# Kernel optimization log

Hardware: AMD Instinct MI355X
Metric: run time of the kernel (lower is better)

## Reference

```python
import jax, jax.numpy as jnp
import numpy as np

D, H, L, P, NQ, B, DFF = 256, 8, 4, 4, 900, 4, 1024
SHAPES = [(128, 128), (64, 64), (32, 32), (16, 16)]
S = sum(h * w for h, w in SHAPES)  # 21760
HD = D // H


def setup_inputs() -> dict:
    key = jax.random.key(0)
    ks = iter(jax.random.split(key, 32))
    r = lambda sh, s=1.0: jax.random.normal(next(ks), sh, jnp.float32) * s
    return dict(
        tgt=r((B, NQ, D)),
        query_pos=r((B, NQ, D)),
        reference_points=jax.random.uniform(next(ks), (B, NQ, L, 2), jnp.float32),
        memory=r((B, S, D)),
        in_proj_w=r((D, 3 * D), 0.02), in_proj_b=jnp.zeros(3 * D, jnp.float32),
        out_proj_w=r((D, D), 0.02), out_proj_b=jnp.zeros(D, jnp.float32),
        ln1_g=jnp.ones(D, jnp.float32), ln1_b=jnp.zeros(D, jnp.float32),
        ln2_g=jnp.ones(D, jnp.float32), ln2_b=jnp.zeros(D, jnp.float32),
        ln3_g=jnp.ones(D, jnp.float32), ln3_b=jnp.zeros(D, jnp.float32),
        vproj_w=r((D, D), 0.02), vproj_b=jnp.zeros(D, jnp.float32),
        off_w=r((D, H * L * P * 2), 0.02), off_b=r((H * L * P * 2,), 0.5),
        aw_w=r((D, H * L * P), 0.02), aw_b=jnp.zeros(H * L * P, jnp.float32),
        oproj_w=r((D, D), 0.02), oproj_b=jnp.zeros(D, jnp.float32),
        lin1_w=r((D, DFF), 0.02), lin1_b=jnp.zeros(DFF, jnp.float32),
        lin2_w=r((DFF, D), 0.02), lin2_b=jnp.zeros(D, jnp.float32),
        spatial_shapes=np.array(SHAPES, np.int32),
        mem_mask=jnp.zeros((B, S), bool),
    )


def _ln(x, g, b):
    m = jnp.mean(x, -1, keepdims=True)
    v = jnp.mean((x - m) ** 2, -1, keepdims=True)
    return (x - m) * jax.lax.rsqrt(v + 1e-5) * g + b


def reference(tgt, query_pos, reference_points, memory,
              in_proj_w, in_proj_b, out_proj_w, out_proj_b,
              ln1_g, ln1_b, ln2_g, ln2_b, ln3_g, ln3_b,
              vproj_w, vproj_b, off_w, off_b, aw_w, aw_b, oproj_w, oproj_b,
              lin1_w, lin1_b, lin2_w, lin2_b, spatial_shapes, mem_mask):
    shapes = np.asarray(spatial_shapes)  # static level shapes

    # ---- self attention (nn.MultiheadAttention, q=k=tgt+pos, v=tgt) ----
    qp = tgt + query_pos
    q = qp @ in_proj_w[:, :D] + in_proj_b[:D]
    k = qp @ in_proj_w[:, D:2 * D] + in_proj_b[D:2 * D]
    v = tgt @ in_proj_w[:, 2 * D:] + in_proj_b[2 * D:]
    split = lambda x: x.reshape(B, NQ, H, HD).transpose(0, 2, 1, 3)
    qh, kh, vh = split(q), split(k), split(v)
    att = jax.nn.softmax(jnp.einsum('bhqd,bhkd->bhqk', qh, kh) / np.sqrt(HD).astype(np.float32), -1)
    sa = jnp.einsum('bhqk,bhkd->bhqd', att, vh).transpose(0, 2, 1, 3).reshape(B, NQ, D)
    tgt = _ln(tgt + sa @ out_proj_w + out_proj_b, ln2_g, ln2_b)

    # ---- MSDeformAttn cross attention ----
    query = tgt + query_pos
    value = memory @ vproj_w + vproj_b
    value = jnp.where(mem_mask[..., None], 0.0, value).reshape(B, S, H, HD)
    off = (query @ off_w + off_b).reshape(B, NQ, H, L, P, 2)
    aw = jax.nn.softmax((query @ aw_w + aw_b).reshape(B, NQ, H, L * P), -1).reshape(B, NQ, H, L, P)
    # offset normalizer is (W_l, H_l)
    normalizer = jnp.stack([jnp.asarray(shapes[:, 1]), jnp.asarray(shapes[:, 0])], -1).astype(jnp.float32)
    loc = reference_points[:, :, None, :, None, :] + off / normalizer[None, None, None, :, None, :]

    acc = jnp.zeros((B, NQ, H, HD), tgt.dtype)
    start = 0
    bidx = jnp.arange(B)[:, None, None, None]
    hidx = jnp.arange(H)[None, None, :, None]
    for l in range(L):
        Hl, Wl = int(shapes[l, 0]), int(shapes[l, 1])
        vf = value[:, start:start + Hl * Wl]  # [B, Hl*Wl, H, HD]
        # grid_sample align_corners=False, zero padding: pixel = loc*size - 0.5
        x = loc[:, :, :, l, :, 0] * Wl - 0.5  # [B,NQ,H,P]
        y = loc[:, :, :, l, :, 1] * Hl - 0.5
        x0 = jnp.floor(x); y0 = jnp.floor(y)
        wx = x - x0; wy = y - y0
        x0i = x0.astype(jnp.int32); y0i = y0.astype(jnp.int32)

        def gather(xi, yi):
            valid = (xi >= 0) & (xi < Wl) & (yi >= 0) & (yi < Hl)
            idx = jnp.clip(yi, 0, Hl - 1) * Wl + jnp.clip(xi, 0, Wl - 1)
            g = vf[bidx, idx, hidx]  # [B,NQ,H,P,HD]
            return jnp.where(valid[..., None], g, 0.0)

        samp = (gather(x0i, y0i) * ((1 - wx) * (1 - wy))[..., None]
                + gather(x0i + 1, y0i) * (wx * (1 - wy))[..., None]
                + gather(x0i, y0i + 1) * ((1 - wx) * wy)[..., None]
                + gather(x0i + 1, y0i + 1) * (wx * wy)[..., None])
        acc = acc + (samp * aw[:, :, :, l, :, None]).sum(3)
        start += Hl * Wl

    ca = acc.reshape(B, NQ, D) @ oproj_w + oproj_b
    tgt = _ln(tgt + ca, ln1_g, ln1_b)

    # ---- FFN ----
    ff = jax.nn.relu(tgt @ lin1_w + lin1_b) @ lin2_w + lin2_b
    return _ln(tgt + ff, ln3_g, ln3_b)
```

## Files before the change

kernel.cpp:

```cpp
#include <hip/hip_runtime.h>
#include <hip/hip_bf16.h>

typedef __attribute__((ext_vector_type(8))) short bf16x8;
typedef __attribute__((ext_vector_type(4))) short bf16x4;
typedef __attribute__((ext_vector_type(4))) float f32x4;

#define DEV static __device__ __forceinline__

constexpr int Bc = 4, NQc = 900, Hc = 8, Sc = 21760;
constexpr int M1 = Bc * NQc;
constexpr int NQT = (NQc + 63) / 64;
constexpr int QT16 = (NQc + 15) / 16;
constexpr int QKo = Bc * Hc * 960 * 32;

DEV short f2bf(float f) {
  union { __hip_bfloat16 h; short s; } u;
  u.h = __float2bfloat16(f);
  return u.s;
}
DEV float bf2f(short s) {
  union { short s; __hip_bfloat16 h; } u;
  u.s = s;
  return __bfloat162float(u.h);
}

DEV void pack_body(const float* W, short* Wt, int K, int N, int t) {
  int n = t % N;
  int k4 = (t / N) * 4;
  bf16x4 o;
  o[0] = f2bf(W[(size_t)(k4 + 0) * N + n]);
  o[1] = f2bf(W[(size_t)(k4 + 1) * N + n]);
  o[2] = f2bf(W[(size_t)(k4 + 2) * N + n]);
  o[3] = f2bf(W[(size_t)(k4 + 3) * N + n]);
  *(bf16x4*)&Wt[((size_t)(k4 >> 5) * N + n) * 32 + (k4 & 31)] = o;
}

__global__ __launch_bounds__(256) void pack_all_k(
    const float* w0, short* t0, const float* w1, short* t1,
    const float* w2, short* t2, const float* w3, short* t3,
    const float* w4, short* t4, const float* w5, short* t5) {
  int t = blockIdx.x * 256 + threadIdx.x;
  if (t < 49152) pack_body(w0, t0, 256, 768, t);
  else if (t < 65536) pack_body(w1, t1, 256, 256, t - 49152);
  else if (t < 81920) pack_body(w2, t2, 256, 256, t - 65536);
  else if (t < 98304) pack_body(w3, t3, 256, 256, t - 81920);
  else if (t < 163840) pack_body(w4, t4, 256, 1024, t - 98304);
  else pack_body(w5, t5, 1024, 256, t - 163840);
}

template <int MODE, int ACT, int MT>
__global__ __launch_bounds__(256) void gemmv_k(
    const float* __restrict__ A, const float* __restrict__ A2,
    const short* __restrict__ Wt, const float* __restrict__ bias,
    void* __restrict__ Cv, float* __restrict__ C2, int M, int N, int K,
    const unsigned char* __restrict__ rowmask, const float* __restrict__ g,
    const float* __restrict__ beta, const float* __restrict__ resid,
    const float* __restrict__ qpos, float* __restrict__ out2) {
  constexpr int IT = MT / 16;
  __shared__ short As[MT * 40];
  __shared__ short Ws[256 * 40];
  const int nb = N >> 8;
  const int mb = blockIdx.x / nb, bn = blockIdx.x - mb * nb;
  const int tid = threadIdx.x;
  const int lane = tid & 63, wave = tid >> 6;
  const int l16 = lane & 15, quad = lane >> 4;
  const int sr = (MT == 64) ? (tid >> 2) : (tid >> 3);
  const int sk = (MT == 64) ? ((tid & 3) * 8) : ((tid & 7) * 4);
  const int arow = mb * MT + sr;
  const bool aval = arow < M;
  const bool useA2 = (MODE == 4) ? (bn < 2) : (A2 != nullptr);
  const float* ap = A + (size_t)arow * K + sk;
  const float* ap2 = (A2 ? A2 : A) + (size_t)arow * K + sk;
  const short* wp = Wt + (size_t)(bn * 256 + tid) * 32;
  const size_t wstep = (size_t)N * 32;
  const int KT = K >> 5;

  f32x4 acc[IT][4] = {};
  float4 pa0[2] = {}, pa1[2] = {};
  bf16x8 pw[2][4];

  auto loadA = [&](int s, int it) {
    if (aval) {
      const float* p = ap + it * 32;
      pa0[s] = *(const float4*)p;
      if constexpr (MT == 64) pa1[s] = *(const float4*)(p + 4);
      if (useA2) {
        const float* p2 = ap2 + it * 32;
        float4 q0 = *(const float4*)p2;
        pa0[s].x += q0.x; pa0[s].y += q0.y; pa0[s].z += q0.z; pa0[s].w += q0.w;
        if constexpr (MT == 64) {
          float4 q1 = *(const float4*)(p2 + 4);
          pa1[s].x += q1.x; pa1[s].y += q1.y; pa1[s].z += q1.z; pa1[s].w += q1.w;
        }
      }
    }
  };
  auto loadW = [&](int s, int it) {
    const short* p = wp + (size_t)it * wstep;
    pw[s][0] = *(const bf16x8*)(p + 0);
    pw[s][1] = *(const bf16x8*)(p + 8);
    pw[s][2] = *(const bf16x8*)(p + 16);
    pw[s][3] = *(const bf16x8*)(p + 24);
  };
  auto stage = [&](int s) {
    if constexpr (MT == 64) {
      bf16x8 t;
      t[0] = f2bf(pa0[s].x); t[1] = f2bf(pa0[s].y); t[2] = f2bf(pa0[s].z); t[3] = f2bf(pa0[s].w);
      t[4] = f2bf(pa1[s].x); t[5] = f2bf(pa1[s].y); t[6] = f2bf(pa1[s].z); t[7] = f2bf(pa1[s].w);
      *(bf16x8*)&As[sr * 40 + sk] = t;
    } else {
      bf16x4 t;
      t[0] = f2bf(pa0[s].x); t[1] = f2bf(pa0[s].y); t[2] = f2bf(pa0[s].z); t[3] = f2bf(pa0[s].w);
      *(bf16x4*)&As[sr * 40 + sk] = t;
    }
    short* wd = &Ws[tid * 40];
    *(bf16x8*)(wd + 0) = pw[s][0];
    *(bf16x8*)(wd + 8) = pw[s][1];
    *(bf16x8*)(wd + 16) = pw[s][2];
    *(bf16x8*)(wd + 24) = pw[s][3];
  };
  auto compute = [&]() {
    bf16x8 af[IT], bfr[4];
#pragma unroll
    for (int i = 0; i < IT; i++)
      af[i] = *(const bf16x8*)&As[(i * 16 + l16) * 40 + quad * 8];
#pragma unroll
    for (int j = 0; j < 4; j++)
      bfr[j] = *(const bf16x8*)&Ws[(wave * 64 + j * 16 + l16) * 40 + quad * 8];
#pragma unroll
    for (int i = 0; i < IT; i++)
#pragma unroll
      for (int j = 0; j < 4; j++)
        acc[i][j] = __builtin_amdgcn_mfma_f32_16x16x32_bf16(af[i], bfr[j], acc[i][j], 0, 0, 0);
  };

  loadA(0, 0); loadW(0, 0);
  loadA(1, 1); loadW(1, 1);
  for (int it = 0; it < KT; it += 2) {
    stage(0);
    __syncthreads();
    if (it + 2 < KT) { loadA(0, it + 2); loadW(0, it + 2); }
    compute();
    __syncthreads();
    stage(1);
    __syncthreads();
    if (it + 3 < KT) { loadA(1, it + 3); loadW(1, it + 3); }
    compute();
    __syncthreads();
  }

  if constexpr (MODE == 4) {
    short* base = (short*)Cv;
#pragma unroll
    for (int i = 0; i < IT; i++)
#pragma unroll
      for (int r = 0; r < 4; r++) {
        const int m = mb * MT + i * 16 + quad * 4 + r;
        if (m >= M) continue;
        const int b = m / NQc, q = m - b * NQc;
#pragma unroll
        for (int j = 0; j < 4; j++) {
          const int cl = wave * 64 + j * 16 + l16;
          const float v = acc[i][j][r] + bias[bn * 256 + cl];
          const int h = cl >> 5, ch = cl & 31;
          if (bn == 0) {
            base[((size_t)(b * 8 + h) * 960 + q) * 32 + ch] =
                f2bf(v * 0.17677669529663687f);
          } else if (bn == 1) {
            base[QKo + ((size_t)(b * 8 + h) * 960 + q) * 32 + ch] = f2bf(v);
          } else {
            base[2 * QKo + ((((size_t)(b * 8 + h) * 15 + (q >> 6)) * 32 + ch) * 64 + (q & 63))] = f2bf(v);
          }
        }
      }
  } else if constexpr (MODE == 0) {
#pragma unroll
    for (int i = 0; i < IT; i++)
#pragma unroll
      for (int j = 0; j < 4; j++) {
        const int cl = wave * 64 + j * 16 + l16;
        const int col = bn * 256 + cl;
        const float bb = bias[col];
#pragma unroll
        for (int r = 0; r < 4; r++) {
          const int m = mb * MT + i * 16 + quad * 4 + r;
          if (m < M) {
            float v = acc[i][j][r] + bb;
            if (ACT == 1) v = fmaxf(v, 0.f);
            ((float*)Cv)[(size_t)m * N + col] = v;
          }
        }
      }
  } else {
#pragma unroll
    for (int j = 0; j < 4; j++) {
      const int cl = wave * 64 + j * 16 + l16;
      const float bb = bias[cl];
#pragma unroll
      for (int i = 0; i < IT; i++)
#pragma unroll
        for (int r = 0; r < 4; r++) {
          const int m = mb * MT + i * 16 + quad * 4 + r;
          const float rs = (m < M) ? resid[(size_t)m * 256 + cl] : 0.f;
          acc[i][j][r] += bb + rs;
        }
    }
    float2* pr = (float2*)As;
#pragma unroll
    for (int i = 0; i < IT; i++)
#pragma unroll
      for (int r = 0; r < 4; r++) {
        float s = 0.f, q = 0.f;
#pragma unroll
        for (int j = 0; j < 4; j++) {
          s += acc[i][j][r];
          q += acc[i][j][r] * acc[i][j][r];
        }
#pragma unroll
        for (int d = 1; d < 16; d <<= 1) {
          s += __shfl_xor(s, d);
          q += __shfl_xor(q, d);
        }
        if (l16 == 0) pr[(i * 16 + quad * 4 + r) * 4 + wave] = make_float2(s, q);
      }
    __syncthreads();
#pragma unroll
    for (int i = 0; i < IT; i++)
#pragma unroll
      for (int r = 0; r < 4; r++) {
        const int ml = i * 16 + quad * 4 + r;
        float2 p0 = pr[ml * 4 + 0], p1 = pr[ml * 4 + 1];
        float2 p2 = pr[ml * 4 + 2], p3 = pr[ml * 4 + 3];
        const float sum = p0.x + p1.x + p2.x + p3.x;
        const float sq = p0.y + p1.y + p2.y + p3.y;
        const float mean = sum * (1.f / 256.f);
        const float var = sq * (1.f / 256.f) - mean * mean;
        const float rstd = rsqrtf(var + 1e-5f);
        const int m = mb * MT + ml;
        if (m < M) {
#pragma unroll
          for (int j = 0; j < 4; j++) {
            const int cl = wave * 64 + j * 16 + l16;
            const float o = (acc[i][j][r] - mean) * rstd * g[cl] + beta[cl];
            ((float*)Cv)[(size_t)m * 256 + cl] = o;
            if (out2) out2[(size_t)m * 256 + cl] = o + qpos[(size_t)m * 256 + cl];
          }
        }
      }
  }
}

__global__ __launch_bounds__(256) void gemm_val_k(
    const float* __restrict__ A, const short* __restrict__ Wt,
    const float* __restrict__ bias, short* __restrict__ Cv, int M,
    const unsigned char* __restrict__ rowmask) {
  const int mb = blockIdx.x;
  const int tid = threadIdx.x;
  const int lane = tid & 63, wave = tid >> 6;
  const int l16 = lane & 15, quad = lane >> 4;

  const float* ap = A + (size_t)(mb * 64 + l16) * 256 + quad * 8;
  const short* wp = Wt + (size_t)(wave * 64 + l16) * 32 + quad * 8;

  f32x4 acc[4][4] = {};
  float4 pa[2][4][2];
  bf16x8 pb[2][4];

  auto loadA = [&](int s, int it) {
#pragma unroll
    for (int i = 0; i < 4; i++) {
      const float* p = ap + (size_t)i * (16 * 256) + it * 32;
      pa[s][i][0] = *(const float4*)p;
      pa[s][i][1] = *(const float4*)(p + 4);
    }
  };
  auto loadB = [&](int s, int it) {
#pragma unroll
    for (int j = 0; j < 4; j++)
      pb[s][j] = *(const bf16x8*)(wp + (size_t)(it * 256 + j * 16) * 32);
  };
  auto comp = [&](int s) {
    bf16x8 af[4];
#pragma unroll
    for (int i = 0; i < 4; i++) {
      af[i][0] = f2bf(pa[s][i][0].x);
      af[i][1] = f2bf(pa[s][i][0].y);
      af[i][2] = f2bf(pa[s][i][0].z);
      af[i][3] = f2bf(pa[s][i][0].w);
      af[i][4] = f2bf(pa[s][i][1].x);
      af[i][5] = f2bf(pa[s][i][1].y);
      af[i][6] = f2bf(pa[s][i][1].z);
      af[i][7] = f2bf(pa[s][i][1].w);
    }
#pragma unroll
    for (int i = 0; i < 4; i++)
#pragma unroll
      for (int j = 0; j < 4; j++)
        acc[i][j] = __builtin_amdgcn_mfma_f32_16x16x32_bf16(af[i], pb[s][j], acc[i][j], 0, 0, 0);
  };

  loadA(0, 0); loadB(0, 0);
  loadA(1, 1); loadB(1, 1);
#pragma unroll
  for (int it = 0; it < 8; it += 2) {
    comp(0);
    if (it + 2 < 8) { loadA(0, it + 2); loadB(0, it + 2); }
    comp(1);
    if (it + 3 < 8) { loadA(1, it + 3); loadB(1, it + 3); }
  }

  float bb[4];
#pragma unroll
  for (int j = 0; j < 4; j++) bb[j] = bias[wave * 64 + j * 16 + l16];
#pragma unroll
  for (int i = 0; i < 4; i++)
#pragma unroll
    for (int r = 0; r < 4; r++) {
      const int m = mb * 64 + i * 16 + quad * 4 + r;
      if (m >= M) continue;
      const bool mk = rowmask[m] != 0;
#pragma unroll
      for (int j = 0; j < 4; j++) {
        const int cl = wave * 64 + j * 16 + l16;
        float v = acc[i][j][r] + bb[j];
        if (mk) v = 0.f;
        Cv[(size_t)m * 256 + cl] = f2bf(v);
      }
    }
}

DEV void gemm32_body(const float* __restrict__ A, const float* __restrict__ W,
                     const float* __restrict__ bias, float* __restrict__ C,
                     int M, int N, int K, int bid) {
  __shared__ float Asf[16][64];
  __shared__ float Bsf[16][68];
  const int nb = N >> 6;
  const int bm = bid / nb, bn = bid % nb;
  const int tid = threadIdx.x;
  const int tm = tid >> 4, tn = tid & 15;
  float acc[4][4] = {};

  for (int k0 = 0; k0 < K; k0 += 16) {
    {
      const int m = tid >> 2, kk = (tid & 3) * 4;
      const int row = bm * 64 + m;
      float4 v = (row < M) ? *(const float4*)(A + (size_t)row * K + k0 + kk)
                           : make_float4(0.f, 0.f, 0.f, 0.f);
      Asf[kk + 0][m] = v.x; Asf[kk + 1][m] = v.y;
      Asf[kk + 2][m] = v.z; Asf[kk + 3][m] = v.w;
    }
    {
      const int kk = tid >> 4, n = (tid & 15) * 4;
      float4 v = *(const float4*)(W + (size_t)(k0 + kk) * N + bn * 64 + n);
      *(float4*)&Bsf[kk][n] = v;
    }
    __syncthreads();
#pragma unroll
    for (int kk = 0; kk < 16; kk++) {
      float a[4], b[4];
#pragma unroll
      for (int i = 0; i < 4; i++) a[i] = Asf[kk][tm * 4 + i];
#pragma unroll
      for (int j = 0; j < 4; j++) b[j] = Bsf[kk][tn * 4 + j];
#pragma unroll
      for (int i = 0; i < 4; i++)
#pragma unroll
        for (int j = 0; j < 4; j++) acc[i][j] = fmaf(a[i], b[j], acc[i][j]);
    }
    __syncthreads();
  }
#pragma unroll
  for (int i = 0; i < 4; i++) {
    const int row = bm * 64 + tm * 4 + i;
    if (row >= M) continue;
#pragma unroll
    for (int j = 0; j < 4; j++) {
      const int col = bn * 64 + tn * 4 + j;
      C[(size_t)row * N + col] = acc[i][j] + bias[col];
    }
  }
}

__global__ __launch_bounds__(256) void gemm32_offaw_k(
    const float* __restrict__ query, const float* __restrict__ off_w,
    const float* __restrict__ off_b, float* __restrict__ offb,
    const float* __restrict__ aw_w, const float* __restrict__ aw_b,
    float* __restrict__ awlin) {
  if (blockIdx.x < 228)
    gemm32_body(query, off_w, off_b, offb, M1, 256, 256, blockIdx.x);
  else
    gemm32_body(query, aw_w, aw_b, awlin, M1, 128, 256, blockIdx.x - 228);
}

__global__ __launch_bounds__(128) void attn_k(const short* __restrict__ qbf,
                                              const short* __restrict__ kbf,
                                              const short* __restrict__ vtbf,
                                              float* __restrict__ sa) {
  __shared__ short Pb[2][16 * 72];
  __shared__ float Om[2][16][32];
  __shared__ float Ml[2][16][2];
  const int bid = blockIdx.x;
  const int qt = bid % QT16, bh = bid / QT16;
  const int tid = threadIdx.x, lane = tid & 63, wave = tid >> 6;
  const int l16 = lane & 15, quad = lane >> 4;

  const int q_local = min(qt * 16 + l16, NQc - 1);
  const bf16x8 qf = *(const bf16x8*)&qbf[((size_t)bh * 960 + q_local) * 32 + quad * 8];
  const short* kb = kbf + (size_t)bh * 960 * 32;
  const short* vb = vtbf + (size_t)bh * 15 * 32 * 64;

  f32x4 o0 = {}, o1 = {};
  float mrun[4] = {-1e30f, -1e30f, -1e30f, -1e30f};
  float lrun[4] = {0.f, 0.f, 0.f, 0.f};
  short* pw = Pb[wave];

  for (int kt = wave; kt < NQT; kt += 2) {
    const int k0 = kt * 64;
    f32x4 s[4];
#pragma unroll
    for (int st = 0; st < 4; st++) {
      const int key = k0 + st * 16 + l16;
      const bf16x8 kf = *(const bf16x8*)&kb[(size_t)key * 32 + quad * 8];
      f32x4 z = {};
      s[st] = __builtin_amdgcn_mfma_f32_16x16x32_bf16(qf, kf, z, 0, 0, 0);
      if (key >= NQc) { s[st][0] = -1e30f; s[st][1] = -1e30f; s[st][2] = -1e30f; s[st][3] = -1e30f; }
    }
    float mnew[4], alpha[4];
#pragma unroll
    for (int r = 0; r < 4; r++) {
      float mx = fmaxf(fmaxf(s[0][r], s[1][r]), fmaxf(s[2][r], s[3][r]));
#pragma unroll
      for (int d = 1; d < 16; d <<= 1) mx = fmaxf(mx, __shfl_xor(mx, d));
      mnew[r] = fmaxf(mrun[r], mx);
      alpha[r] = __expf(mrun[r] - mnew[r]);
      mrun[r] = mnew[r];
    }
    float tsum[4] = {0.f, 0.f, 0.f, 0.f};
#pragma unroll
    for (int st = 0; st < 4; st++)
#pragma unroll
      for (int r = 0; r < 4; r++) {
        float p = __expf(s[st][r] - mnew[r]);
        s[st][r] = p;
        tsum[r] += p;
      }
#pragma unroll
    for (int r = 0; r < 4; r++) {
      float t = tsum[r];
#pragma unroll
      for (int d = 1; d < 16; d <<= 1) t += __shfl_xor(t, d);
      lrun[r] = lrun[r] * alpha[r] + t;
      o0[r] *= alpha[r];
      o1[r] *= alpha[r];
    }
#pragma unroll
    for (int st = 0; st < 4; st++)
#pragma unroll
      for (int r = 0; r < 4; r++)
        pw[(quad * 4 + r) * 72 + st * 16 + l16] = f2bf(s[st][r]);
    const short* vt = vb + kt * (32 * 64);
#pragma unroll
    for (int c = 0; c < 2; c++) {
      bf16x8 pf = *(const bf16x8*)&pw[l16 * 72 + c * 32 + quad * 8];
      bf16x8 vf0 = *(const bf16x8*)&vt[(size_t)l16 * 64 + c * 32 + quad * 8];
      bf16x8 vf1 = *(const bf16x8*)&vt[(size_t)(16 + l16) * 64 + c * 32 + quad * 8];
      o0 = __builtin_amdgcn_mfma_f32_16x16x32_bf16(pf, vf0, o0, 0, 0, 0);
      o1 = __builtin_amdgcn_mfma_f32_16x16x32_bf16(pf, vf1, o1, 0, 0, 0);
    }
  }
#pragma unroll
  for (int r = 0; r < 4; r++) {
    Om[wave][quad * 4 + r][l16] = o0[r];
    Om[wave][quad * 4 + r][16 + l16] = o1[r];
  }
  if (l16 == 0) {
#pragma unroll
    for (int r = 0; r < 4; r++) {
      Ml[wave][quad * 4 + r][0] = mrun[r];
      Ml[wave][quad * 4 + r][1] = lrun[r];
    }
  }
  __syncthreads();
  {
    const int q = tid >> 3;
    const int c4 = (tid & 7) * 4;
    const float m0 = Ml[0][q][0], m1 = Ml[1][q][0];
    const float M = fmaxf(m0, m1);
    const float a0 = __expf(m0 - M), a1 = __expf(m1 - M);
    const float lsum = a0 * Ml[0][q][1] + a1 * Ml[1][q][1];
    const int qg = qt * 16 + q;
    if (qg < NQc) {
      const float inv = 1.f / lsum;
      float4 o;
      o.x = (a0 * Om[0][q][c4 + 0] + a1 * Om[1][q][c4 + 0]) * inv;
      o.y = (a0 * Om[0][q][c4 + 1] + a1 * Om[1][q][c4 + 1]) * inv;
      o.z = (a0 * Om[0][q][c4 + 2] + a1 * Om[1][q][c4 + 2]) * inv;
      o.w = (a0 * Om[0][q][c4 + 3] + a1 * Om[1][q][c4 + 3]) * inv;
      const int b = bh >> 3, h = bh & 7;
      *(float4*)&sa[(size_t)(b * NQc + qg) * 256 + h * 32 + c4] = o;
    }
  }
}

__global__ __launch_bounds__(256) void sample_k(
    const float* __restrict__ awlin, const float* __restrict__ off,
    const float* __restrict__ refp, const short* __restrict__ value,
    float* __restrict__ accout) {
  const int wid = blockIdx.x * 4 + (threadIdx.x >> 6);
  const int lane = threadIdx.x & 63;
  const int bq = wid >> 3, h = wid & 7;
  const int b = bq / NQc;
  const int l16 = lane & 15;

  float wraw = awlin[(size_t)bq * 128 + h * 16 + l16];
  float mx = wraw;
#pragma unroll
  for (int d = 1; d < 16; d <<= 1) mx = fmaxf(mx, __shfl_xor(mx, d));
  float e = __expf(wraw - mx), ssum = e;
#pragma unroll
  for (int d = 1; d < 16; d <<= 1) ssum += __shfl_xor(ssum, d);
  const float wnorm = e / ssum;

  const int ch = lane & 31, sub = lane >> 5;
  float facc = 0.f;
#pragma unroll
  for (int it = 0; it < 8; it++) {
    const int pt = it * 2 + sub;
    const float w = __shfl(wnorm, pt);
    const int l = pt >> 2;
    const int W = 128 >> l;
    const int start = (l == 0) ? 0 : (l == 1) ? 16384 : (l == 2) ? 20480 : 21504;
    const float offx = off[(size_t)bq * 256 + h * 32 + pt * 2];
    const float offy = off[(size_t)bq * 256 + h * 32 + pt * 2 + 1];
    const float rx = refp[(size_t)bq * 8 + l * 2];
    const float ry = refp[(size_t)bq * 8 + l * 2 + 1];
    const float x = rx * (float)W + offx - 0.5f;
    const float y = ry * (float)W + offy - 0.5f;
    const float x0f = floorf(x), y0f = floorf(y);
    const float wx = x - x0f, wy = y - y0f;
    const int x0 = (int)x0f, y0 = (int)y0f;
    const short* vbp = value + ((size_t)b * Sc + start) * 256 + h * 32 + ch;
#pragma unroll
    for (int c4 = 0; c4 < 4; c4++) {
      const int dx = c4 & 1, dy = c4 >> 1;
      const int xi = x0 + dx, yi = y0 + dy;
      const bool valid = (xi >= 0) && (xi < W) && (yi >= 0) && (yi < W);
      const int xc = min(max(xi, 0), W - 1);
      const int yc = min(max(yi, 0), W - 1);
      const float gvv = bf2f(vbp[(size_t)(yc * W + xc) * 256]);
      const float ww = (dx ? wx : 1.f - wx) * (dy ? wy : 1.f - wy);
      facc += valid ? w * ww * gvv : 0.f;
    }
  }
  facc += __shfl_xor(facc, 32);
  if (lane < 32) accout[(size_t)bq * 256 + h * 32 + ch] = facc;
}

extern "C" void kernel_launch(void* const* d_in, const int* in_sizes, int n_in,
                              void* d_out, int out_size, void* d_ws,
                              size_t ws_size, hipStream_t stream) {
  const float* tgt = (const float*)d_in[0];
  const float* query_pos = (const float*)d_in[1];
  const float* refp = (const float*)d_in[2];
  const float* memory = (const float*)d_in[3];
  const float* in_proj_w = (const float*)d_in[4];
  const float* in_proj_b = (const float*)d_in[5];
  const float* out_proj_w = (const float*)d_in[6];
  const float* out_proj_b = (const float*)d_in[7];
  const float* ln1_g = (const float*)d_in[8];
  const float* ln1_b = (const float*)d_in[9];
  const float* ln2_g = (const float*)d_in[10];
  const float* ln2_b = (const float*)d_in[11];
  const float* ln3_g = (const float*)d_in[12];
  const float* ln3_b = (const float*)d_in[13];
  const float* vproj_w = (const float*)d_in[14];
  const float* vproj_b = (const float*)d_in[15];
  const float* off_w = (const float*)d_in[16];
  const float* off_b = (const float*)d_in[17];
  const float* aw_w = (const float*)d_in[18];
  const float* aw_b = (const float*)d_in[19];
  const float* oproj_w = (const float*)d_in[20];
  const float* oproj_b = (const float*)d_in[21];
  const float* lin1_w = (const float*)d_in[22];
  const float* lin1_b = (const float*)d_in[23];
  const float* lin2_w = (const float*)d_in[24];
  const float* lin2_b = (const float*)d_in[25];
  const unsigned char* mem_mask = (const unsigned char*)d_in[27];
  float* out = (float*)d_out;

  float* ws = (float*)d_ws;
  short* qbf = (short*)(ws + 921600);
  float* sa = ws + 3686400;
  float* tgt2 = ws + 5529600;
  float* query = ws + 6451200;
  float* offb = ws + 7372800;
  float* awlin = ws + 8294400;
  float* accb = ws + 8755200;
  float* tgt3 = ws + 9676800;
  float* ff1 = ws + 10598400;
  short* valueBf = (short*)(ws + 14284800);
  short* wbase = valueBf + 22282240;
  short* inT = wbase + 0;
  short* outT = wbase + 196608;
  short* vT = wbase + 262144;
  short* oT = wbase + 327680;
  short* lin1T = wbase + 393216;
  short* lin2T = wbase + 655360;

  pack_all_k<<<896, 256, 0, stream>>>(in_proj_w, inT, out_proj_w, outT,
                                      vproj_w, vT, oproj_w, oT,
                                      lin1_w, lin1T, lin2_w, lin2T);

  gemmv_k<4, 0, 32><<<113 * 3, 256, 0, stream>>>(
      tgt, query_pos, inT, in_proj_b, qbf, nullptr, M1, 768, 256,
      nullptr, nullptr, nullptr, nullptr, nullptr, nullptr);
  attn_k<<<Bc * Hc * QT16, 128, 0, stream>>>(qbf, qbf + QKo, qbf + 2 * QKo, sa);
  gemmv_k<3, 0, 32><<<113, 256, 0, stream>>>(
      sa, nullptr, outT, out_proj_b, tgt2, nullptr, M1, 256, 256,
      nullptr, ln2_g, ln2_b, tgt, query_pos, query);
  gemm_val_k<<<1360, 256, 0, stream>>>(memory, vT, vproj_b, valueBf, Bc * Sc, mem_mask);
  gemm32_offaw_k<<<342, 256, 0, stream>>>(query, off_w, off_b, offb, aw_w, aw_b, awlin);
  sample_k<<<Bc * NQc * Hc / 4, 256, 0, stream>>>(awlin, offb, refp, valueBf, accb);
  gemmv_k<3, 0, 32><<<113, 256, 0, stream>>>(
      accb, nullptr, oT, oproj_b, tgt3, nullptr, M1, 256, 256,
      nullptr, ln1_g, ln1_b, tgt2, nullptr, nullptr);
  gemmv_k<0, 1, 64><<<57 * 4, 256, 0, stream>>>(
      tgt3, nullptr, lin1T, lin1_b, ff1, nullptr, M1, 1024, 256,
      nullptr, nullptr, nullptr, nullptr, nullptr, nullptr);
  gemmv_k<3, 0, 32><<<113, 256, 0, stream>>>(
      ff1, nullptr, lin2T, lin2_b, out, nullptr, M1, 256, 1024,
      nullptr, ln3_g, ln3_b, tgt3, nullptr, nullptr);
}
```

Measured before the change: 422.7 us.

## Stage value-projection A tiles into LDS via async global_load_lds with N split

Rewrites the value-projection GEMM so fp32 memory rows are copied directly into a double-buffered, XOR-swizzled LDS tile using global_load_lds, rather than each wave loading them into registers. The N dimension is split across two blocks with a 2x2 wave layout, which doubles the grid and halves the accumulators per wave. An occupancy hint of 4 blocks is added. The aim is to lower register pressure and redundant A traffic and to overlap copies with MFMA work. The cost is syncthreads barriers on every iteration, and each A tile is now read by two blocks.

```diff
diff --git a/kernel.cpp b/kernel.cpp
--- a/kernel.cpp
+++ b/kernel.cpp
@@ -250,28 +250,35 @@
   }
 }
 
-__global__ __launch_bounds__(256) void gemm_val_k(
+__global__ __launch_bounds__(256, 4) void gemm_val_k(
     const float* __restrict__ A, const short* __restrict__ Wt,
     const float* __restrict__ bias, short* __restrict__ Cv, int M,
     const unsigned char* __restrict__ rowmask) {
-  const int mb = blockIdx.x;
+  __shared__ float As[2][64 * 32];
+  const int mb = blockIdx.x >> 1, bn = blockIdx.x & 1;
   const int tid = threadIdx.x;
   const int lane = tid & 63, wave = tid >> 6;
   const int l16 = lane & 15, quad = lane >> 4;
-
-  const float* ap = A + (size_t)(mb * 64 + l16) * 256 + quad * 8;
-  const short* wp = Wt + (size_t)(wave * 64 + l16) * 32 + quad * 8;
-
-  f32x4 acc[4][4] = {};
-  float4 pa[2][4][2];
+  const int wr = wave & 1, wc = wave >> 1;
+
+  const short* wp = Wt + (size_t)(bn * 128 + wc * 64 + l16) * 32 + quad * 8;
+
+  const int srow_lo = lane >> 3;
+  const int schunk = ((lane & 7) ^ srow_lo) * 4;
+  const float* abase =
+      A + (size_t)(mb * 64 + wave * 8 + srow_lo) * 256 + schunk;
+
+  f32x4 acc[2][4] = {};
   bf16x8 pb[2][4];
 
-  auto loadA = [&](int s, int it) {
-#pragma unroll
-    for (int i = 0; i < 4; i++) {
-      const float* p = ap + (size_t)i * (16 * 256) + it * 32;
-      pa[s][i][0] = *(const float4*)p;
-      pa[s][i][1] = *(const float4*)(p + 4);
+  auto stage = [&](int buf, int it) {
+#pragma unroll
+    for (int call = 0; call < 2; ++call) {
+      const float* src = abase + (size_t)call * (32 * 256) + it * 32;
+      float* dst = &As[buf][(call * 32 + wave * 8) * 32];
+      __builtin_amdgcn_global_load_lds(
+          (const __attribute__((address_space(1))) void*)src,
+          (__attribute__((address_space(3))) void*)dst, 16, 0, 0);
     }
   };
   auto loadB = [&](int s, int it) {
@@ -279,49 +286,51 @@
     for (int j = 0; j < 4; j++)
       pb[s][j] = *(const bf16x8*)(wp + (size_t)(it * 256 + j * 16) * 32);
   };
-  auto comp = [&](int s) {
-    bf16x8 af[4];
-#pragma unroll
-    for (int i = 0; i < 4; i++) {
-      af[i][0] = f2bf(pa[s][i][0].x);
-      af[i][1] = f2bf(pa[s][i][0].y);
-      af[i][2] = f2bf(pa[s][i][0].z);
-      af[i][3] = f2bf(pa[s][i][0].w);
-      af[i][4] = f2bf(pa[s][i][1].x);
-      af[i][5] = f2bf(pa[s][i][1].y);
-      af[i][6] = f2bf(pa[s][i][1].z);
-      af[i][7] = f2bf(pa[s][i][1].w);
-    }
-#pragma unroll
-    for (int i = 0; i < 4; i++)
+  auto compute = [&](int cur) {
+    bf16x8 af[2];
+#pragma unroll
+    for (int i = 0; i < 2; i++) {
+      const int row = wr * 32 + i * 16 + l16;
+      const int cb = row & 7;
+      const float4 a0 =
+          *(const float4*)&As[cur][row * 32 + (((quad * 2) ^ cb) << 2)];
+      const float4 a1 =
+          *(const float4*)&As[cur][row * 32 + (((quad * 2 + 1) ^ cb) << 2)];
+      af[i][0] = f2bf(a0.x); af[i][1] = f2bf(a0.y);
+      af[i][2] = f2bf(a0.z); af[i][3] = f2bf(a0.w);
+      af[i][4] = f2bf(a1.x); af[i][5] = f2bf(a1.y);
+      af[i][6] = f2bf(a1.z); af[i][7] = f2bf(a1.w);
+    }
+#pragma unroll
+    for (int i = 0; i < 2; i++)
 #pragma unroll
       for (int j = 0; j < 4; j++)
-        acc[i][j] = __builtin_amdgcn_mfma_f32_16x16x32_bf16(af[i], pb[s][j], acc[i][j], 0, 0, 0);
+        acc[i][j] = __builtin_amdgcn_mfma_f32_16x16x32_bf16(af[i], pb[cur][j],
+                                                            acc[i][j], 0, 0, 0);
   };
 
-  loadA(0, 0); loadB(0, 0);
-  loadA(1, 1); loadB(1, 1);
-#pragma unroll
-  for (int it = 0; it < 8; it += 2) {
-    comp(0);
-    if (it + 2 < 8) { loadA(0, it + 2); loadB(0, it + 2); }
-    comp(1);
-    if (it + 3 < 8) { loadA(1, it + 3); loadB(1, it + 3); }
+  stage(0, 0);
+  loadB(0, 0);
+  __syncthreads();
+  for (int it = 0; it < 8; ++it) {
+    const int cur = it & 1;
+    if (it + 1 < 8) { stage(cur ^ 1, it + 1); loadB(cur ^ 1, it + 1); }
+    compute(cur);
+    __syncthreads();
   }
 
   float bb[4];
 #pragma unroll
-  for (int j = 0; j < 4; j++) bb[j] = bias[wave * 64 + j * 16 + l16];
-#pragma unroll
-  for (int i = 0; i < 4; i++)
+  for (int j = 0; j < 4; j++) bb[j] = bias[bn * 128 + wc * 64 + j * 16 + l16];
+#pragma unroll
+  for (int i = 0; i < 2; i++)
 #pragma unroll
     for (int r = 0; r < 4; r++) {
-      const int m = mb * 64 + i * 16 + quad * 4 + r;
-      if (m >= M) continue;
+      const int m = mb * 64 + wr * 32 + i * 16 + quad * 4 + r;
       const bool mk = rowmask[m] != 0;
 #pragma unroll
       for (int j = 0; j < 4; j++) {
-        const int cl = wave * 64 + j * 16 + l16;
+        const int cl = bn * 128 + wc * 64 + j * 16 + l16;
         float v = acc[i][j][r] + bb[j];
         if (mk) v = 0.f;
         Cv[(size_t)m * 256 + cl] = f2bf(v);
@@ -618,7 +627,7 @@
   gemmv_k<3, 0, 32><<<113, 256, 0, stream>>>(
       sa, nullptr, outT, out_proj_b, tgt2, nullptr, M1, 256, 256,
       nullptr, ln2_g, ln2_b, tgt, query_pos, query);
-  gemm_val_k<<<1360, 256, 0, stream>>>(memory, vT, vproj_b, valueBf, Bc * Sc, mem_mask);
+  gemm_val_k<<<2720, 256, 0, stream>>>(memory, vT, vproj_b, valueBf, Bc * Sc, mem_mask);
   gemm32_offaw_k<<<342, 256, 0, stream>>>(query, off_w, off_b, offb, aw_w, aw_b, awlin);
   sample_k<<<Bc * NQc * Hc / 4, 256, 0, stream>>>(awlin, offb, refp, valueBf, accb);
   gemmv_k<3, 0, 32><<<113, 256, 0, stream>>>(
```

After: 403.2 us. -4.6%, faster.
